# Performance work log

Measured on AMD Instinct MI355X. Metric: run time of the kernel, lower is better.

Reference implementation:

```python
import jax, jax.numpy as jnp
import numpy as np

B, T, X, Y, H = 256, 1024, 64, 64, 256


def setup_inputs() -> dict:
    key = jax.random.key(0)
    ks = jax.random.split(key, 7)
    inputs = jax.random.normal(ks[0], (B, T, X + Y), dtype=jnp.float32)
    # zero out the last quarter of timesteps so Masking(mask_value=0.0) is exercised
    tmask = (jnp.arange(T) < (3 * T) // 4).astype(jnp.float32)[None, :, None]
    inputs = inputs * tmask
    s = 0.05
    return {
        "inputs": inputs,
        "W_enc": jax.random.normal(ks[1], (X + Y, 4 * H), dtype=jnp.float32) * s,
        "U_enc": jax.random.normal(ks[2], (H, 4 * H), dtype=jnp.float32) * s,
        "b_enc": jnp.zeros((4 * H,), dtype=jnp.float32),
        "W_dec": jax.random.normal(ks[3], (X + H, 4 * H), dtype=jnp.float32) * s,
        "U_dec": jax.random.normal(ks[4], (H, 4 * H), dtype=jnp.float32) * s,
        "b_dec": jnp.zeros((4 * H,), dtype=jnp.float32),
        "W_out": jax.random.normal(ks[5], (H, Y), dtype=jnp.float32) * s,
        "b_out": jnp.zeros((Y,), dtype=jnp.float32),
        "x_dim": X,
    }


def _lstm_relu(xW_t, U, mask_t=None, return_seq=False):
    """Keras LSTM with activation='relu', recurrent_activation='sigmoid'.
    xW_t: [T,B,4H] precomputed x@W + b. mask_t: optional [T,B] bool.
    Gate order i, f, c, o (Keras). Masked steps carry (h, c) through.
    """
    Hn = U.shape[0]
    Bn = xW_t.shape[1]
    h0 = jnp.zeros((Bn, Hn), dtype=xW_t.dtype)
    c0 = jnp.zeros((Bn, Hn), dtype=xW_t.dtype)

    def step(carry, inp):
        h, c = carry
        if mask_t is None:
            xw = inp
        else:
            xw, m = inp
        z = xw + h @ U                       # [B,4H]
        i, f, g, o = jnp.split(z, 4, axis=-1)
        i = jax.nn.sigmoid(i)
        f = jax.nn.sigmoid(f)
        o = jax.nn.sigmoid(o)
        g = jax.nn.relu(g)                   # activation='relu'
        c_new = f * c + i * g
        h_new = o * jax.nn.relu(c_new)       # activation='relu' on cell output
        if mask_t is not None:
            mm = m[:, None]
            h_new = jnp.where(mm, h_new, h)
            c_new = jnp.where(mm, c_new, c)
        return (h_new, c_new), (h_new if return_seq else None)

    xs = xW_t if mask_t is None else (xW_t, mask_t)
    (h_fin, _), hs = jax.lax.scan(step, (h0, c0), xs)
    return h_fin, hs


def reference(inputs, W_enc, U_enc, b_enc, W_dec, U_dec, b_dec, W_out, b_out, x_dim):
    # Masking(mask_value=0.0): timestep valid iff any feature != 0
    mask = jnp.any(inputs != 0.0, axis=-1)                 # [B,T]
    # Encoder LSTM, return_sequences=False
    xW = jnp.einsum('bti,ij->btj', inputs, W_enc) + b_enc  # [B,T,4H]
    h_fin, _ = _lstm_relu(xW.transpose(1, 0, 2), U_enc,
                          mask_t=mask.T, return_seq=False)  # [B,H]
    # RepeatVector + concat with x part
    Tn = inputs.shape[1]
    latent_rep = jnp.broadcast_to(h_fin[:, None, :], (h_fin.shape[0], Tn, h_fin.shape[1]))
    dec_inp = jnp.concatenate([inputs[:, :, :x_dim], latent_rep], axis=-1)  # [B,T,X+H]
    # Decoder LSTM, return_sequences=True (no mask)
    xW2 = jnp.einsum('bti,ij->btj', dec_inp, W_dec) + b_dec
    _, hs = _lstm_relu(xW2.transpose(1, 0, 2), U_dec, mask_t=None, return_seq=True)  # [T,B,H]
    hs = hs.transpose(1, 0, 2)                              # [B,T,H]
    # TimeDistributed Dense(y_dim)
    return jnp.einsum('bth,hy->bty', hs, W_out) + b_out
```

## Files before the change

### kernel.cpp

```cpp
#include <hip/hip_runtime.h>


typedef __bf16 bf16x8 __attribute__((ext_vector_type(8)));
typedef float f32x4 __attribute__((ext_vector_type(4)));
typedef unsigned int uint4v __attribute__((ext_vector_type(4)));
typedef unsigned long long ull;

#define DI __device__ __forceinline__

DI unsigned short f2bf(float f) {
  unsigned int u = __float_as_uint(f);
  u += 0x7fffu + ((u >> 16) & 1u);
  return (unsigned short)(u >> 16);
}
DI float sigf(float v) { return 1.0f / (1.0f + __expf(-v)); }

union FragU { bf16x8 v; unsigned short us[8]; };
union H8 { bf16x8 v; ull u[2]; uint4v q; };

DI f32x4 mfma16(bf16x8 a, bf16x8 b, f32x4 c) {
  return __builtin_amdgcn_mfma_f32_16x16x32_bf16(a, b, c, 0, 0, 0);
}

__global__ void pack_frags(const float* __restrict__ src,
                           unsigned short* __restrict__ dst, int K, int N) {
  int KT = K >> 5, NT = N >> 4;
  int total = KT * NT * 64;
  for (int idx = blockIdx.x * blockDim.x + threadIdx.x; idx < total;
       idx += gridDim.x * blockDim.x) {
    int lane = idx & 63;
    int fi = idx >> 6;
    int nt = fi % NT;
    int kt = fi / NT;
    int r0 = kt * 32 + (lane >> 4) * 8;
    int col = nt * 16 + (lane & 15);
    unsigned int w[4];
#pragma unroll
    for (int p = 0; p < 4; ++p) {
      unsigned int lo = f2bf(src[(size_t)(r0 + 2 * p) * N + col]);
      unsigned int hi = f2bf(src[(size_t)(r0 + 2 * p + 1) * N + col]);
      w[p] = lo | (hi << 16);
    }
    *(uint4v*)(dst + (size_t)idx * 8) = (uint4v){w[0], w[1], w[2], w[3]};
  }
}

__global__ void mask_flags(const float* __restrict__ x,
                           unsigned int* __restrict__ fmask) {
  const int t = blockIdx.x;
  const int b = threadIdx.x;
  const float* p = x + ((size_t)b * 1024 + t) * 128;
  bool nz = false;
#pragma unroll 8
  for (int k = 0; k < 32; ++k) {
    float4 v = *(const float4*)(p + k * 4);
    nz = nz || v.x != 0.f || v.y != 0.f || v.z != 0.f || v.w != 0.f;
  }
  unsigned long long bal = __ballot((int)nz);
  if ((threadIdx.x & 15) == 0)
    fmask[(size_t)(b >> 4) * 1024 + t] =
        (unsigned int)((bal >> (threadIdx.x & 48)) & 0xFFFFull);
}

#define LOAD_ULDS(SRC) do {                                                 \
    _Pragma("unroll")                                                       \
    for (int vv = 0; vv < 32; ++vv) {                                       \
      int flat = vv * 256 + tid;                                            \
      int kt_ = flat >> 10, ntl = (flat >> 6) & 15, ln = flat & 63;         \
      int nt_ = (ntl >> 2) * 16 + s * 4 + (ntl & 3);                        \
      ((uint4v*)ulds)[flat] = ((const uint4v*)(SRC))[(kt_ * 64 + nt_) * 64 + ln]; \
    } } while (0)

#define EXCHANGE(HX, FLAG, TIDX) do {                                       \
    __syncthreads();                                                        \
    if (tid == 0) {                                                         \
      __hip_atomic_fetch_add(&(FLAG)[g * 1024 + (TIDX)], 1u,                \
                             __ATOMIC_RELEASE, __HIP_MEMORY_SCOPE_AGENT);   \
      unsigned it = 0;                                                      \
      while (__hip_atomic_load(&(FLAG)[g * 1024 + (TIDX)],                  \
                 __ATOMIC_RELAXED, __HIP_MEMORY_SCOPE_AGENT) < 4u) {        \
        __builtin_amdgcn_s_sleep(1);                                        \
        if (++it > (1u << 16)) break;                                       \
      }                                                                     \
    }                                                                       \
    __syncthreads();                                                        \
    const ull* hxr = (const ull*)((HX) + ((size_t)g * 2 + pb) * 4096);      \
    _Pragma("unroll")                                                       \
    for (int kt_ = 0; kt_ < 8; ++kt_) {                                     \
      H8 hh_;                                                               \
      hh_.u[0] = __hip_atomic_load(&hxr[(kt_ * 64 + lane) * 2],             \
                     __ATOMIC_RELAXED, __HIP_MEMORY_SCOPE_AGENT);           \
      hh_.u[1] = __hip_atomic_load(&hxr[(kt_ * 64 + lane) * 2 + 1],         \
                     __ATOMIC_RELAXED, __HIP_MEMORY_SCOPE_AGENT);           \
      hfr[kt_] = hh_.v;                                                     \
    }                                                                       \
    pb ^= 1;                                                                \
  } while (0)

__global__ __launch_bounds__(256) __attribute__((amdgpu_waves_per_eu(1, 1)))
void enc_rnn(const float* __restrict__ x,
             const unsigned short* __restrict__ Wef,
             const unsigned short* __restrict__ Uef,
             const float* __restrict__ benc,
             const unsigned int* __restrict__ fmask,
             unsigned short* __restrict__ hxE,
             unsigned int* __restrict__ flagE,
             unsigned short* __restrict__ hfin) {
  __shared__ __align__(16) unsigned short ulds[8 * 16 * 64 * 8];

  const int tid = threadIdx.x;
  const int w = tid >> 6, lane = tid & 63;
  const int l15 = lane & 15, lkg = lane >> 4;
  const int bid = blockIdx.x;
  const int s = bid >> 4, g = bid & 15;
  const int b0 = g * 16;
  int ntf[4];
#pragma unroll
  for (int G = 0; G < 4; ++G) ntf[G] = G * 16 + s * 4 + w;

  LOAD_ULDS(Uef);

  const bf16x8* Wl = (const bf16x8*)Wef + lane;
  bf16x8 wpin[4][4];
#pragma unroll
  for (int G = 0; G < 4; ++G)
#pragma unroll
    for (int kt = 0; kt < 4; ++kt) wpin[G][kt] = Wl[(kt * 64 + ntf[G]) * 64];

  float bfr[4];
#pragma unroll
  for (int G = 0; G < 4; ++G) bfr[G] = benc[ntf[G] * 16 + l15];

  float c4[4];
  unsigned short hreg[4];
  bf16x8 hfr[8];
#pragma unroll
  for (int q = 0; q < 4; ++q) { c4[q] = 0.f; hreg[q] = 0; }
  H8 z_; z_.u[0] = 0; z_.u[1] = 0;
#pragma unroll
  for (int kt = 0; kt < 8; ++kt) hfr[kt] = z_.v;

  const float* xbase = x + (size_t)(b0 + l15) * 1024 * 128 + lkg * 8;
  const unsigned int* flagp = fmask + (size_t)g * 1024;
  const int ktst = 2 * s + (w >> 1);
  const int lbase = (w & 1) * 32 + (l15 >> 3) * 16 + lkg * 4;
  const int jst = l15 & 7;
  int pb = 0;

  __syncthreads();

  for (int t = 0; t < 1024; ++t) {
    const unsigned int flag_t = flagp[t];
    if (flag_t == 0u) continue;

    const float* xp = xbase + (size_t)t * 128;
    float4 xa[4][2];
#pragma unroll
    for (int kt = 0; kt < 4; ++kt) {
      xa[kt][0] = *(const float4*)(xp + kt * 32);
      xa[kt][1] = *(const float4*)(xp + kt * 32 + 4);
    }

    f32x4 acc[4];
#pragma unroll
    for (int G = 0; G < 4; ++G) acc[G] = (f32x4){bfr[G], bfr[G], bfr[G], bfr[G]};

#pragma unroll
    for (int kt = 0; kt < 8; ++kt)
#pragma unroll
      for (int G = 0; G < 4; ++G) {
        bf16x8 u_ = *(const bf16x8*)&ulds[(size_t)(((kt * 16 + G * 4 + w) * 64 + lane)) * 8];
        acc[G] = mfma16(hfr[kt], u_, acc[G]);
      }

    FragU xf[4];
#pragma unroll
    for (int kt = 0; kt < 4; ++kt) {
      xf[kt].us[0] = f2bf(xa[kt][0].x); xf[kt].us[1] = f2bf(xa[kt][0].y);
      xf[kt].us[2] = f2bf(xa[kt][0].z); xf[kt].us[3] = f2bf(xa[kt][0].w);
      xf[kt].us[4] = f2bf(xa[kt][1].x); xf[kt].us[5] = f2bf(xa[kt][1].y);
      xf[kt].us[6] = f2bf(xa[kt][1].z); xf[kt].us[7] = f2bf(xa[kt][1].w);
    }
#pragma unroll
    for (int kt = 0; kt < 4; ++kt)
#pragma unroll
      for (int G = 0; G < 4; ++G) acc[G] = mfma16(xf[kt].v, wpin[G][kt], acc[G]);

    unsigned short* hxw = hxE + ((size_t)g * 2 + pb) * 4096;
#pragma unroll
    for (int q = 0; q < 4; ++q) {
      float iv = sigf(acc[0][q]);
      float fv = sigf(acc[1][q]);
      float gv = fmaxf(acc[2][q], 0.f);
      float ov = sigf(acc[3][q]);
      float cn = fv * c4[q] + iv * gv;
      float hn = ov * fmaxf(cn, 0.f);
      bool m = (flag_t >> (lkg * 4 + q)) & 1u;
      c4[q] = m ? cn : c4[q];
      unsigned short hh = m ? f2bf(hn) : hreg[q];
      hreg[q] = hh;
      __hip_atomic_store(&hxw[(ktst * 64 + lbase + q) * 8 + jst], hh,
                         __ATOMIC_RELAXED, __HIP_MEMORY_SCOPE_AGENT);
    }

    EXCHANGE(hxE, flagE, t);
  }

  if (w < 2) {
    int kt = 2 * s + w;
    H8 hh_; hh_.v = hfr[kt];
    *(uint4v*)&hfin[((size_t)g * 8 + kt) * 512 + lane * 8] = hh_.q;
  }
}

__global__ __launch_bounds__(256) __attribute__((amdgpu_waves_per_eu(1, 1)))
void dec_rnn(const float* __restrict__ x,
             const unsigned short* __restrict__ Wd0f,
             const unsigned short* __restrict__ WdLf,
             const unsigned short* __restrict__ Udf,
             const float* __restrict__ bdec,
             const unsigned short* __restrict__ Wof,
             const float* __restrict__ bout,
             const unsigned short* __restrict__ hfin,
             unsigned short* __restrict__ hxD,
             unsigned int* __restrict__ flagD,
             float* __restrict__ out) {
  __shared__ __align__(16) unsigned short ulds[8 * 16 * 64 * 8];

  const int tid = threadIdx.x;
  const int w = tid >> 6, lane = tid & 63;
  const int l15 = lane & 15, lkg = lane >> 4;
  const int bid = blockIdx.x;
  const int s = bid >> 4, g = bid & 15;
  const int b0 = g * 16;
  int ntf[4];
#pragma unroll
  for (int G = 0; G < 4; ++G) ntf[G] = G * 16 + s * 4 + w;

  LOAD_ULDS(Udf);

  const bf16x8* W0l = (const bf16x8*)Wd0f + lane;
  const bf16x8* WLl = (const bf16x8*)WdLf + lane;
  bf16x8 w0pin[4][2];
#pragma unroll
  for (int G = 0; G < 4; ++G)
#pragma unroll
    for (int kt = 0; kt < 2; ++kt) w0pin[G][kt] = W0l[(kt * 64 + ntf[G]) * 64];

  f32x4 lat[4];
  {
    bf16x8 ha[8];
#pragma unroll
    for (int kt = 0; kt < 8; ++kt)
      ha[kt] = *(const bf16x8*)&hfin[((size_t)g * 8 + kt) * 512 + lane * 8];
#pragma unroll
    for (int G = 0; G < 4; ++G) {
      float bd = bdec[ntf[G] * 16 + l15];
      lat[G] = (f32x4){bd, bd, bd, bd};
    }
#pragma unroll
    for (int kt = 0; kt < 8; ++kt)
#pragma unroll
      for (int G = 0; G < 4; ++G)
        lat[G] = mfma16(ha[kt], WLl[(kt * 64 + ntf[G]) * 64], lat[G]);
  }

  bf16x8 wofr[8];
  if (w == 0) {
#pragma unroll
    for (int kt = 0; kt < 8; ++kt)
      wofr[kt] = ((const bf16x8*)Wof)[(kt * 4 + s) * 64 + lane];
  }
  const float bo = bout[s * 16 + l15];

  float c4[4];
  bf16x8 hfr[8];
#pragma unroll
  for (int q = 0; q < 4; ++q) c4[q] = 0.f;
  H8 z_; z_.u[0] = 0; z_.u[1] = 0;
#pragma unroll
  for (int kt = 0; kt < 8; ++kt) hfr[kt] = z_.v;

  const float* xbase = x + (size_t)(b0 + l15) * 1024 * 128 + lkg * 8;
  const int ktst = 2 * s + (w >> 1);
  const int lbase = (w & 1) * 32 + (l15 >> 3) * 16 + lkg * 4;
  const int jst = l15 & 7;
  int pb = 0;

  __syncthreads();

  for (int t = 0; t < 1024; ++t) {
    const float* xp = xbase + (size_t)t * 128;
    float4 xa[2][2];
#pragma unroll
    for (int kt = 0; kt < 2; ++kt) {
      xa[kt][0] = *(const float4*)(xp + kt * 32);
      xa[kt][1] = *(const float4*)(xp + kt * 32 + 4);
    }

    f32x4 acc[4];
#pragma unroll
    for (int G = 0; G < 4; ++G) acc[G] = lat[G];

#pragma unroll
    for (int kt = 0; kt < 8; ++kt)
#pragma unroll
      for (int G = 0; G < 4; ++G) {
        bf16x8 u_ = *(const bf16x8*)&ulds[(size_t)(((kt * 16 + G * 4 + w) * 64 + lane)) * 8];
        acc[G] = mfma16(hfr[kt], u_, acc[G]);
      }

    FragU xf[2];
#pragma unroll
    for (int kt = 0; kt < 2; ++kt) {
      xf[kt].us[0] = f2bf(xa[kt][0].x); xf[kt].us[1] = f2bf(xa[kt][0].y);
      xf[kt].us[2] = f2bf(xa[kt][0].z); xf[kt].us[3] = f2bf(xa[kt][0].w);
      xf[kt].us[4] = f2bf(xa[kt][1].x); xf[kt].us[5] = f2bf(xa[kt][1].y);
      xf[kt].us[6] = f2bf(xa[kt][1].z); xf[kt].us[7] = f2bf(xa[kt][1].w);
    }
#pragma unroll
    for (int kt = 0; kt < 2; ++kt)
#pragma unroll
      for (int G = 0; G < 4; ++G) acc[G] = mfma16(xf[kt].v, w0pin[G][kt], acc[G]);

    unsigned short* hxw = hxD + ((size_t)g * 2 + pb) * 4096;
#pragma unroll
    for (int q = 0; q < 4; ++q) {
      float iv = sigf(acc[0][q]);
      float fv = sigf(acc[1][q]);
      float gv = fmaxf(acc[2][q], 0.f);
      float ov = sigf(acc[3][q]);
      float cn = fv * c4[q] + iv * gv;
      float hn = ov * fmaxf(cn, 0.f);
      c4[q] = cn;
      __hip_atomic_store(&hxw[(ktst * 64 + lbase + q) * 8 + jst], f2bf(hn),
                         __ATOMIC_RELAXED, __HIP_MEMORY_SCOPE_AGENT);
    }

    EXCHANGE(hxD, flagD, t);

    if (w == 0) {
      f32x4 oa = {bo, bo, bo, bo};
#pragma unroll
      for (int kt = 0; kt < 8; ++kt) oa = mfma16(hfr[kt], wofr[kt], oa);
#pragma unroll
      for (int q = 0; q < 4; ++q)
        out[((size_t)(b0 + lkg * 4 + q) * 1024 + t) * 64 + s * 16 + l15] = oa[q];
    }
  }
}

extern "C" void kernel_launch(void* const* d_in, const int* in_sizes, int n_in,
                              void* d_out, int out_size, void* d_ws, size_t ws_size,
                              hipStream_t stream) {
  const float* inputs = (const float*)d_in[0];
  const float* W_enc  = (const float*)d_in[1];
  const float* U_enc  = (const float*)d_in[2];
  const float* b_enc  = (const float*)d_in[3];
  const float* W_dec  = (const float*)d_in[4];
  const float* U_dec  = (const float*)d_in[5];
  const float* b_dec  = (const float*)d_in[6];
  const float* W_out  = (const float*)d_in[7];
  const float* b_out  = (const float*)d_in[8];

  char* ws = (char*)d_ws;
  unsigned short* Uef   = (unsigned short*)(ws + 0);
  unsigned short* Udf   = (unsigned short*)(ws + 524288);
  unsigned short* Wef   = (unsigned short*)(ws + 1048576);
  unsigned short* Wd0f  = (unsigned short*)(ws + 1310720);
  unsigned short* WdLf  = (unsigned short*)(ws + 1441792);
  unsigned short* Wof   = (unsigned short*)(ws + 1966080);
  unsigned short* hfin  = (unsigned short*)(ws + 1998848);
  unsigned int*   fmask = (unsigned int*)(ws + 2129920);
  unsigned int*   flagE = (unsigned int*)(ws + 2195456);
  unsigned int*   flagD = (unsigned int*)(ws + 2260992);
  unsigned short* hxE   = (unsigned short*)(ws + 2326528);
  unsigned short* hxD   = (unsigned short*)(ws + 2588672);

  hipMemsetAsync(ws + 2195456, 0, 131072, stream);

  mask_flags<<<1024, 256, 0, stream>>>(inputs, fmask);
  pack_frags<<<128, 256, 0, stream>>>(U_enc, Uef, 256, 1024);
  pack_frags<<<128, 256, 0, stream>>>(U_dec, Udf, 256, 1024);
  pack_frags<<<128, 256, 0, stream>>>(W_enc, Wef, 128, 1024);
  pack_frags<<<128, 256, 0, stream>>>(W_dec, Wd0f, 64, 1024);
  pack_frags<<<128, 256, 0, stream>>>(W_dec + 64 * 1024, WdLf, 256, 1024);
  pack_frags<<<32, 256, 0, stream>>>(W_out, Wof, 256, 64);

  enc_rnn<<<64, 256, 0, stream>>>(inputs, Wef, Uef, b_enc, fmask,
                                  hxE, flagE, hfin);
  dec_rnn<<<64, 256, 0, stream>>>(inputs, Wd0f, WdLf, Udf, b_dec, Wof, b_out,
                                  hfin, hxD, flagD, (float*)d_out);
}
```

Baseline: 6.163 ms.

## Split cross-block exchange into signal/wait and overlap prefetch and output with wait

The old barrier-style exchange is split into a signal phase and a wait phase. The next timestep's input loads and, in the decoder, the previous step's output projection now run between the two, hiding them behind inter-block synchronisation latency. The wait now spins in every thread rather than only thread 0, with no sleep and a shorter timeout. That trades extra polling traffic for lower wake-up latency and risks an early break under contention.

```diff
diff --git a/kernel.cpp b/kernel.cpp
--- a/kernel.cpp
+++ b/kernel.cpp
@@ -71,19 +71,19 @@
       ((uint4v*)ulds)[flat] = ((const uint4v*)(SRC))[(kt_ * 64 + nt_) * 64 + ln]; \
     } } while (0)
 
-#define EXCHANGE(HX, FLAG, TIDX) do {                                       \
+#define EXCH_SIGNAL(FLAG, TIDX) do {                                        \
     __syncthreads();                                                        \
-    if (tid == 0) {                                                         \
+    if (tid == 0)                                                           \
       __hip_atomic_fetch_add(&(FLAG)[g * 1024 + (TIDX)], 1u,                \
                              __ATOMIC_RELEASE, __HIP_MEMORY_SCOPE_AGENT);   \
-      unsigned it = 0;                                                      \
-      while (__hip_atomic_load(&(FLAG)[g * 1024 + (TIDX)],                  \
-                 __ATOMIC_RELAXED, __HIP_MEMORY_SCOPE_AGENT) < 4u) {        \
-        __builtin_amdgcn_s_sleep(1);                                        \
-        if (++it > (1u << 16)) break;                                       \
-      }                                                                     \
+  } while (0)
+
+#define EXCH_WAIT(HX, FLAG, TIDX) do {                                      \
+    unsigned it_ = 0;                                                       \
+    while (__hip_atomic_load(&(FLAG)[g * 1024 + (TIDX)],                    \
+               __ATOMIC_RELAXED, __HIP_MEMORY_SCOPE_AGENT) < 4u) {          \
+      if (++it_ > (1u << 12)) break;                                        \
     }                                                                       \
-    __syncthreads();                                                        \
     const ull* hxr = (const ull*)((HX) + ((size_t)g * 2 + pb) * 4096);      \
     _Pragma("unroll")                                                       \
     for (int kt_ = 0; kt_ < 8; ++kt_) {                                     \
@@ -146,19 +146,22 @@
   const int lbase = (w & 1) * 32 + (l15 >> 3) * 16 + lkg * 4;
   const int jst = l15 & 7;
   int pb = 0;
+  bool xvalid = false;
+  float4 xa[4][2];
 
   __syncthreads();
 
   for (int t = 0; t < 1024; ++t) {
     const unsigned int flag_t = flagp[t];
-    if (flag_t == 0u) continue;
-
-    const float* xp = xbase + (size_t)t * 128;
-    float4 xa[4][2];
-#pragma unroll
-    for (int kt = 0; kt < 4; ++kt) {
-      xa[kt][0] = *(const float4*)(xp + kt * 32);
-      xa[kt][1] = *(const float4*)(xp + kt * 32 + 4);
+    if (flag_t == 0u) { xvalid = false; continue; }
+
+    if (!xvalid) {
+      const float* xp = xbase + (size_t)t * 128;
+#pragma unroll
+      for (int kt = 0; kt < 4; ++kt) {
+        xa[kt][0] = *(const float4*)(xp + kt * 32);
+        xa[kt][1] = *(const float4*)(xp + kt * 32 + 4);
+      }
     }
 
     f32x4 acc[4];
@@ -203,7 +206,19 @@
                          __ATOMIC_RELAXED, __HIP_MEMORY_SCOPE_AGENT);
     }
 
-    EXCHANGE(hxE, flagE, t);
+    EXCH_SIGNAL(flagE, t);
+
+    if (t < 1023) {
+      const float* xq = xbase + (size_t)(t + 1) * 128;
+#pragma unroll
+      for (int kt = 0; kt < 4; ++kt) {
+        xa[kt][0] = *(const float4*)(xq + kt * 32);
+        xa[kt][1] = *(const float4*)(xq + kt * 32 + 4);
+      }
+      xvalid = true;
+    } else xvalid = false;
+
+    EXCH_WAIT(hxE, flagE, t);
   }
 
   if (w < 2) {
@@ -287,17 +302,13 @@
   const int jst = l15 & 7;
   int pb = 0;
 
+  float4 xa[2][2];
+  xa[0][0] = *(const float4*)(xbase);      xa[0][1] = *(const float4*)(xbase + 4);
+  xa[1][0] = *(const float4*)(xbase + 32); xa[1][1] = *(const float4*)(xbase + 36);
+
   __syncthreads();
 
   for (int t = 0; t < 1024; ++t) {
-    const float* xp = xbase + (size_t)t * 128;
-    float4 xa[2][2];
-#pragma unroll
-    for (int kt = 0; kt < 2; ++kt) {
-      xa[kt][0] = *(const float4*)(xp + kt * 32);
-      xa[kt][1] = *(const float4*)(xp + kt * 32 + 4);
-    }
-
     f32x4 acc[4];
 #pragma unroll
     for (int G = 0; G < 4; ++G) acc[G] = lat[G];
@@ -337,16 +348,32 @@
                          __ATOMIC_RELAXED, __HIP_MEMORY_SCOPE_AGENT);
     }
 
-    EXCHANGE(hxD, flagD, t);
-
-    if (w == 0) {
+    EXCH_SIGNAL(flagD, t);
+
+    if (t > 0 && w == 0) {
       f32x4 oa = {bo, bo, bo, bo};
 #pragma unroll
       for (int kt = 0; kt < 8; ++kt) oa = mfma16(hfr[kt], wofr[kt], oa);
 #pragma unroll
       for (int q = 0; q < 4; ++q)
-        out[((size_t)(b0 + lkg * 4 + q) * 1024 + t) * 64 + s * 16 + l15] = oa[q];
-    }
+        out[((size_t)(b0 + lkg * 4 + q) * 1024 + (t - 1)) * 64 + s * 16 + l15] = oa[q];
+    }
+    if (t < 1023) {
+      const float* xq = xbase + (size_t)(t + 1) * 128;
+      xa[0][0] = *(const float4*)(xq);      xa[0][1] = *(const float4*)(xq + 4);
+      xa[1][0] = *(const float4*)(xq + 32); xa[1][1] = *(const float4*)(xq + 36);
+    }
+
+    EXCH_WAIT(hxD, flagD, t);
+  }
+
+  if (w == 0) {
+    f32x4 oa = {bo, bo, bo, bo};
+#pragma unroll
+    for (int kt = 0; kt < 8; ++kt) oa = mfma16(hfr[kt], wofr[kt], oa);
+#pragma unroll
+    for (int q = 0; q < 4; ++q)
+      out[((size_t)(b0 + lkg * 4 + q) * 1024 + 1023) * 64 + s * 16 + l15] = oa[q];
   }
 }
 
```

Result: faster. 5.978 ms (-3.0%).
